# Kernel optimization log

Hardware: AMD Instinct MI355X
Metric: run time of the kernel (lower is better)

Reference implementation:

```python
import jax, jax.numpy as jnp
import numpy as np

D_MODEL = 1024
N_HEADS = 16
HEAD_DIM = D_MODEL // N_HEADS
SCALE = HEAD_DIM ** -0.5
MASK_FILL = -10000.0


def setup_inputs() -> dict:
    key = jax.random.key(0)
    ks = jax.random.split(key, 12)
    B, L, D = 2, 2048, D_MODEL
    inv = 1.0 / np.sqrt(D)
    inp = {
        "query": jax.random.normal(ks[0], (B, L, D), jnp.float32),
        "key": jax.random.normal(ks[1], (B, L, D), jnp.float32),
        "value": jax.random.normal(ks[2], (B, L, D), jnp.float32),
        "Wq": jax.random.normal(ks[3], (D, D), jnp.float32) * inv,
        "bq": jnp.zeros((D,), jnp.float32),
        "Wk": jax.random.normal(ks[4], (D, D), jnp.float32) * inv,
        "bk": jnp.zeros((D,), jnp.float32),
        "Wv": jax.random.normal(ks[5], (D, D), jnp.float32) * inv,
        "bv": jnp.zeros((D,), jnp.float32),
        "Wo": jax.random.normal(ks[6], (D, D), jnp.float32) * inv,
        "bo": jnp.zeros((D,), jnp.float32),
        "valid_mask": jax.random.randint(ks[7], (B, L), 0, 2).astype(jnp.bool_),
    }
    return inp


def reference(query, key, value, Wq, bq, Wk, bk, Wv, bv, Wo, bo, valid_mask):
    B, Lq, D = query.shape
    Lk = key.shape[1]
    H, HD = N_HEADS, HEAD_DIM
    # torch.nn.Linear: y = x @ W.T + b
    Q = (query @ Wq.T + bq).reshape(B, Lq, H, HD).transpose(0, 2, 1, 3)  # [B,H,Lq,HD]
    K = (key @ Wk.T + bk).reshape(B, Lk, H, HD).transpose(0, 2, 1, 3)    # [B,H,Lk,HD]
    V = (value @ Wv.T + bv).reshape(B, Lk, H, HD).transpose(0, 2, 1, 3)  # [B,H,Lk,HD]
    scores = jnp.einsum("bhqd,bhkd->bhqk", Q, K) * SCALE
    scores = jnp.where(valid_mask[:, None, None, :], scores, MASK_FILL)
    weights = jax.nn.softmax(scores, axis=-1)  # dropout is identity at inference
    out = jnp.einsum("bhqk,bhkd->bhqd", weights, V)
    out = out.transpose(0, 2, 1, 3).reshape(B, Lq, D)
    out = out @ Wo.T + bo
    # zero rows of fully-invalid batches
    gate = jnp.any(valid_mask, axis=1).astype(out.dtype)[:, None, None]
    return out * gate
```

## Files before the change

### kernel.cpp

```cpp
#include <hip/hip_runtime.h>
#include <hip/hip_bf16.h>

typedef __hip_bfloat16 bf16;
typedef __attribute__((ext_vector_type(8))) short s8v;
typedef __attribute__((ext_vector_type(4))) float f4v;

#define LOG2E 1.44269504088896340736f
#define CSCALE (0.125f * LOG2E)
#define MASK_B2 (-14426.950408889634f)
#define NEG_BIG (-30000.0f)

#define BB 2
#define LL 2048
#define DD 1024
#define HH 16
#define HD 64
#define MTOT 4096
#define PER_T 4194304

struct alignas(8) B4 { bf16 v[4]; };

__device__ __forceinline__ void async_cp16(const bf16* g, bf16* l) {
    __builtin_amdgcn_global_load_lds(
        (const __attribute__((address_space(1))) void*)g,
        (__attribute__((address_space(3))) void*)l, 16, 0, 0);
}

struct CvtArgs {
    const float* src[7];
    bf16* dst[7];
    int n[7];
};

__global__ __launch_bounds__(256) void cvt_kernel(CvtArgs args) {
    const int which = blockIdx.y;
    const float* __restrict__ src = args.src[which];
    bf16* __restrict__ dst = args.dst[which];
    const int n4 = args.n[which] >> 2;
    const int stride = gridDim.x * 256;
    for (int i = blockIdx.x * 256 + threadIdx.x; i < n4; i += stride) {
        const float4 f = ((const float4*)src)[i];
        B4 o;
        o.v[0] = __float2bfloat16(f.x);
        o.v[1] = __float2bfloat16(f.y);
        o.v[2] = __float2bfloat16(f.z);
        o.v[3] = __float2bfloat16(f.w);
        ((B4*)dst)[i] = o;
    }
}

struct QkvArgs {
    const bf16* A[3];
    const bf16* W[3];
    const float* bias[3];
    bf16* out[3];
};

template <int FUSED>
__global__ __launch_bounds__(256) void gemm128(QkvArgs qa,
                                               const bf16* __restrict__ Ao,
                                               const bf16* __restrict__ Wo_,
                                               const float* __restrict__ bo_,
                                               float* __restrict__ out_f,
                                               const int* __restrict__ mask) {
    __shared__ bf16 sA[128 * 64];
    __shared__ bf16 sB[128 * 64];
    __shared__ int sgate;

    const int which = FUSED ? blockIdx.z : 0;
    const bf16* __restrict__ A = FUSED ? qa.A[which] : Ao;
    const bf16* __restrict__ W = FUSED ? qa.W[which] : Wo_;
    const float* __restrict__ bias = FUSED ? qa.bias[which] : bo_;
    bf16* __restrict__ out_bf = FUSED ? qa.out[which] : nullptr;

    const int lane = threadIdx.x & 63;
    const int w = threadIdx.x >> 6;
    const int lr = lane & 15;
    const int quad = lane >> 4;
    const int wr = w >> 1, wc = w & 1;
    const int rbase = blockIdx.x * 128;
    const int cbase = blockIdx.y * 128;
    const int dma_r = lane >> 3;
    const int dma_cc = ((lane & 7) ^ dma_r) * 8;

    if (!FUSED) {
        if (threadIdx.x == 0) sgate = 0;
        __syncthreads();
        const int b_ = rbase >> 11;
        int any = 0;
        for (int i = threadIdx.x; i < LL; i += 256) any |= mask[b_ * LL + i];
        if (any) sgate = 1;
    }

    f4v acc[4][4] = {};
    for (int kt = 0; kt < DD / 64; kt++) {
        const int k0 = kt * 64;
        __syncthreads();
#pragma unroll
        for (int t = 0; t < 4; t++) {
            const int g = w * 4 + t;
            async_cp16(A + (size_t)(rbase + g * 8 + dma_r) * DD + k0 + dma_cc,
                       &sA[g * 512]);
            async_cp16(W + (size_t)(cbase + g * 8 + dma_r) * DD + k0 + dma_cc,
                       &sB[g * 512]);
        }
        __syncthreads();
#pragma unroll
        for (int s = 0; s < 2; s++) {
            s8v a[4], b[4];
#pragma unroll
            for (int i = 0; i < 4; i++) {
                const int row = wr * 64 + i * 16 + lr;
                a[i] = *(const s8v*)&sA[row * 64 + (((s * 4 + quad) ^ (row & 7)) * 8)];
            }
#pragma unroll
            for (int j = 0; j < 4; j++) {
                const int row = wc * 64 + j * 16 + lr;
                b[j] = *(const s8v*)&sB[row * 64 + (((s * 4 + quad) ^ (row & 7)) * 8)];
            }
#pragma unroll
            for (int i = 0; i < 4; i++)
#pragma unroll
                for (int j = 0; j < 4; j++)
                    acc[i][j] = __builtin_amdgcn_mfma_f32_16x16x32_bf16(a[i], b[j], acc[i][j], 0, 0, 0);
        }
    }

    const float gatef = (!FUSED) ? (sgate ? 1.0f : 0.0f) : 1.0f;

#pragma unroll
    for (int j = 0; j < 4; j++) {
        const int n = cbase + wc * 64 + j * 16 + lr;
        const float bv = bias[n];
#pragma unroll
        for (int i = 0; i < 4; i++) {
#pragma unroll
            for (int r = 0; r < 4; r++) {
                const int m = rbase + wr * 64 + i * 16 + quad * 4 + r;
                const float v = acc[i][j][r] + bv;
                if (!FUSED) {
                    out_f[(size_t)m * DD + n] = v * gatef;
                } else {
                    const int b_ = m >> 11, l = m & (LL - 1);
                    const int h = n >> 6, hd = n & 63;
                    if (which == 2)
                        out_bf[(((size_t)(b_ * HH + h)) * HD + hd) * LL + l] = __float2bfloat16(v);
                    else
                        out_bf[(((size_t)(b_ * HH + h)) * LL + l) * HD + hd] = __float2bfloat16(v);
                }
            }
        }
    }
}

__global__ __launch_bounds__(256) void attn_kernel(const bf16* __restrict__ Q,
                                                   const bf16* __restrict__ K,
                                                   const bf16* __restrict__ Vt,
                                                   const int* __restrict__ mask,
                                                   bf16* __restrict__ Aout) {
    __shared__ bf16 sK[2][64 * 64];
    __shared__ bf16 sV[2][64 * 64];
    __shared__ bf16 sP[4][16 * 72];
    __shared__ float sBias[LL];

    const int lane = threadIdx.x & 63;
    const int w = threadIdx.x >> 6;
    const int lr = lane & 15;
    const int quad = lane >> 4;

    const int bid = blockIdx.x;
    const int qb = bid & 31;
    const int h = (bid >> 5) & 15;
    const int b = bid >> 9;

    const size_t head_off = ((size_t)(b * HH + h)) * LL * HD;
    const bf16* Qh = Q + head_off;
    const bf16* Kh = K + head_off;
    const bf16* Vh = Vt + head_off;
    const int q0 = qb * 64 + w * 16;

    const int dma_r = lane >> 3;
    const int dma_cc = ((lane & 7) ^ dma_r) * 8;
    const int sw = lr & 7;

    {
        const int* mb = mask + b * LL;
        for (int i = threadIdx.x; i < LL; i += 256)
            sBias[i] = mb[i] ? 0.0f : MASK_B2;
#pragma unroll
        for (int t = 0; t < 2; t++) {
            const int g = w * 2 + t;
            async_cp16(Kh + (size_t)(g * 8 + dma_r) * HD + dma_cc, &sK[0][g * 512]);
            async_cp16(Vh + (size_t)(g * 8 + dma_r) * LL + dma_cc, &sV[0][g * 512]);
        }
    }
    __syncthreads();

    const s8v aq0 = *(const s8v*)(Qh + (size_t)(q0 + lr) * HD + quad * 8);
    const s8v aq1 = *(const s8v*)(Qh + (size_t)(q0 + lr) * HD + 32 + quad * 8);

    bf16* sPw = &sP[w][0];
    f4v O[4] = {};
    float mrun = NEG_BIG, lrun = 0.0f;

    int asrc[4];
#pragma unroll
    for (int r = 0; r < 4; r++) asrc[r] = (lane & 48) | (quad * 4 + r);

    for (int kt = 0; kt < LL / 64; kt++) {
        const int kbase = kt * 64;
        const bf16* kb = &sK[kt & 1][0];
        const bf16* vb = &sV[kt & 1][0];

        if (kt < LL / 64 - 1) {
            const int nb = (kt + 1) & 1;
#pragma unroll
            for (int t = 0; t < 2; t++) {
                const int g = w * 2 + t;
                async_cp16(Kh + (size_t)(kbase + 64 + g * 8 + dma_r) * HD + dma_cc,
                           &sK[nb][g * 512]);
                async_cp16(Vh + (size_t)(g * 8 + dma_r) * LL + kbase + 64 + dma_cc,
                           &sV[nb][g * 512]);
            }
        }

        f4v T[4];
#pragma unroll
        for (int j = 0; j < 4; j++) {
            const int row = 16 * j + lr;
            const s8v kb0 = *(const s8v*)&kb[row * 64 + ((quad ^ sw) * 8)];
            const s8v kb1 = *(const s8v*)&kb[row * 64 + (((quad + 4) ^ sw) * 8)];
            f4v t = {};
            t = __builtin_amdgcn_mfma_f32_16x16x32_bf16(kb0, aq0, t, 0, 0, 0);
            T[j] = __builtin_amdgcn_mfma_f32_16x16x32_bf16(kb1, aq1, t, 0, 0, 0);
        }

        s8v v0[4], v1[4];
#pragma unroll
        for (int dt = 0; dt < 4; dt++) {
            const int vrow = dt * 16 + lr;
            v0[dt] = *(const s8v*)&vb[vrow * 64 + ((quad ^ sw) * 8)];
            v1[dt] = *(const s8v*)&vb[vrow * 64 + (((quad + 4) ^ sw) * 8)];
        }

        float mloc = NEG_BIG;
#pragma unroll
        for (int j = 0; j < 4; j++) {
            const f4v bj = *(const f4v*)&sBias[kbase + j * 16 + quad * 4];
#pragma unroll
            for (int r = 0; r < 4; r++) {
                T[j][r] = T[j][r] * CSCALE + bj[r];
                mloc = fmaxf(mloc, T[j][r]);
            }
        }
        mloc = fmaxf(mloc, __shfl_xor(mloc, 16));
        mloc = fmaxf(mloc, __shfl_xor(mloc, 32));

        if (__any(mloc > mrun)) {
            const float mnew = fmaxf(mrun, mloc);
            const float alphaq = exp2f(mrun - mnew);
            mrun = mnew;
            lrun *= alphaq;
            float aB[4];
#pragma unroll
            for (int r = 0; r < 4; r++) aB[r] = __shfl(alphaq, asrc[r]);
#pragma unroll
            for (int dt = 0; dt < 4; dt++)
#pragma unroll
                for (int r = 0; r < 4; r++) O[dt][r] *= aB[r];
        }

        float ls = 0.0f;
#pragma unroll
        for (int j = 0; j < 4; j++)
#pragma unroll
            for (int r = 0; r < 4; r++) {
                const float e = exp2f(T[j][r] - mrun);
                T[j][r] = e;
                ls += e;
            }
        ls += __shfl_xor(ls, 16);
        ls += __shfl_xor(ls, 32);
        lrun += ls;

        asm volatile("" ::: "memory");
#pragma unroll
        for (int j = 0; j < 4; j++) {
            B4 pk;
            pk.v[0] = __float2bfloat16(T[j][0]);
            pk.v[1] = __float2bfloat16(T[j][1]);
            pk.v[2] = __float2bfloat16(T[j][2]);
            pk.v[3] = __float2bfloat16(T[j][3]);
            *(B4*)&sPw[lr * 72 + j * 16 + quad * 4] = pk;
        }
        asm volatile("s_waitcnt lgkmcnt(0)" ::: "memory");
        const s8v pa0 = *(const s8v*)(sPw + lr * 72 + quad * 8);
        const s8v pa1 = *(const s8v*)(sPw + lr * 72 + 32 + quad * 8);

#pragma unroll
        for (int dt = 0; dt < 4; dt++) {
            O[dt] = __builtin_amdgcn_mfma_f32_16x16x32_bf16(pa0, v0[dt], O[dt], 0, 0, 0);
            O[dt] = __builtin_amdgcn_mfma_f32_16x16x32_bf16(pa1, v1[dt], O[dt], 0, 0, 0);
        }

        __syncthreads();
    }

    const float linv = 1.0f / lrun;
    float lB[4];
#pragma unroll
    for (int r = 0; r < 4; r++) lB[r] = __shfl(linv, asrc[r]);
#pragma unroll
    for (int dt = 0; dt < 4; dt++)
#pragma unroll
        for (int r = 0; r < 4; r++) {
            const int q = q0 + quad * 4 + r;
            Aout[((size_t)(b * LL + q)) * DD + h * HD + dt * 16 + lr] =
                __float2bfloat16(O[dt][r] * lB[r]);
        }
}

extern "C" void kernel_launch(void* const* d_in, const int* in_sizes, int n_in,
                              void* d_out, int out_size, void* d_ws, size_t ws_size,
                              hipStream_t stream) {
    const float* query = (const float*)d_in[0];
    const float* key   = (const float*)d_in[1];
    const float* value = (const float*)d_in[2];
    const float* Wq = (const float*)d_in[3];
    const float* bq = (const float*)d_in[4];
    const float* Wk = (const float*)d_in[5];
    const float* bk = (const float*)d_in[6];
    const float* Wv = (const float*)d_in[7];
    const float* bv = (const float*)d_in[8];
    const float* Wo = (const float*)d_in[9];
    const float* bo = (const float*)d_in[10];
    const int* mask = (const int*)d_in[11];

    bf16* base = (bf16*)d_ws;
    bf16* qx = base;
    bf16* kx = qx + PER_T;
    bf16* vx = kx + PER_T;
    bf16* wq = vx + PER_T;
    bf16* wk = wq + DD * DD;
    bf16* wv = wk + DD * DD;
    bf16* wo = wv + DD * DD;
    bf16* Qs = wo + DD * DD;
    bf16* Ks = Qs + PER_T;
    bf16* Vst = Ks + PER_T;
    bf16* aws = Vst + PER_T;

    CvtArgs ca;
    ca.src[0] = query; ca.dst[0] = qx; ca.n[0] = PER_T;
    ca.src[1] = key;   ca.dst[1] = kx; ca.n[1] = PER_T;
    ca.src[2] = value; ca.dst[2] = vx; ca.n[2] = PER_T;
    ca.src[3] = Wq;    ca.dst[3] = wq; ca.n[3] = DD * DD;
    ca.src[4] = Wk;    ca.dst[4] = wk; ca.n[4] = DD * DD;
    ca.src[5] = Wv;    ca.dst[5] = wv; ca.n[5] = DD * DD;
    ca.src[6] = Wo;    ca.dst[6] = wo; ca.n[6] = DD * DD;
    cvt_kernel<<<dim3(1024, 7), 256, 0, stream>>>(ca);

    QkvArgs qa;
    qa.A[0] = qx; qa.W[0] = wq; qa.bias[0] = bq; qa.out[0] = Qs;
    qa.A[1] = kx; qa.W[1] = wk; qa.bias[1] = bk; qa.out[1] = Ks;
    qa.A[2] = vx; qa.W[2] = wv; qa.bias[2] = bv; qa.out[2] = Vst;

    gemm128<1><<<dim3(MTOT / 128, DD / 128, 3), 256, 0, stream>>>(
        qa, nullptr, nullptr, nullptr, nullptr, nullptr);

    attn_kernel<<<BB * HH * (LL / 64), 256, 0, stream>>>(Qs, Ks, Vst, mask, aws);

    QkvArgs dummy{};
    gemm128<0><<<dim3(MTOT / 128, DD / 128, 1), 256, 0, stream>>>(
        dummy, aws, wo, bo, (float*)d_out, mask);
}
```

Before: 293.6 us.

## Split attention keys across waves with register-resident P and smaller output GEMM tiles

The attention kernel now has each wave handle all 64 queries against a 16-key slice of every key tile, instead of 16 queries against all keys. Probabilities stay in registers and feed 16x16x16 MFMAs directly, removing the shared-memory round trip for P. The per-wave softmax states are merged at the end through shared memory using LDS atomics before writing bf16 output. The output projection GEMM switches to 64-row tiles to launch more blocks, at the cost of more accumulators per wave in attention and an extra reduction step.

```diff
diff --git a/kernel.cpp b/kernel.cpp
--- a/kernel.cpp
+++ b/kernel.cpp
@@ -3,6 +3,7 @@
 
 typedef __hip_bfloat16 bf16;
 typedef __attribute__((ext_vector_type(8))) short s8v;
+typedef __attribute__((ext_vector_type(4))) short s4v;
 typedef __attribute__((ext_vector_type(4))) float f4v;
 
 #define LOG2E 1.44269504088896340736f
@@ -24,6 +25,16 @@
     __builtin_amdgcn_global_load_lds(
         (const __attribute__((address_space(1))) void*)g,
         (__attribute__((address_space(3))) void*)l, 16, 0, 0);
+}
+
+__device__ __forceinline__ f4v mfma16x16x16bf(s4v a, s4v b, f4v c) {
+    return __builtin_amdgcn_mfma_f32_16x16x16bf16_1k(a, b, c, 0, 0, 0);
+}
+
+__device__ __forceinline__ unsigned pk2(float lo, float hi) {
+    unsigned a = __builtin_bit_cast(unsigned, hi) + 0x8000u;
+    unsigned b = __builtin_bit_cast(unsigned, lo) + 0x8000u;
+    return __builtin_amdgcn_perm(a, b, 0x07060302u);
 }
 
 struct CvtArgs {
@@ -56,16 +67,17 @@
     bf16* out[3];
 };
 
-template <int FUSED>
+template <int FUSED, int MT>
 __global__ __launch_bounds__(256) void gemm128(QkvArgs qa,
                                                const bf16* __restrict__ Ao,
                                                const bf16* __restrict__ Wo_,
                                                const float* __restrict__ bo_,
                                                float* __restrict__ out_f,
                                                const int* __restrict__ mask) {
-    __shared__ bf16 sA[128 * 64];
+    __shared__ bf16 sA[MT * 64];
     __shared__ bf16 sB[128 * 64];
     __shared__ int sgate;
+    constexpr int NI = MT / 32;
 
     const int which = FUSED ? blockIdx.z : 0;
     const bf16* __restrict__ A = FUSED ? qa.A[which] : Ao;
@@ -78,7 +90,7 @@
     const int lr = lane & 15;
     const int quad = lane >> 4;
     const int wr = w >> 1, wc = w & 1;
-    const int rbase = blockIdx.x * 128;
+    const int rbase = blockIdx.x * MT;
     const int cbase = blockIdx.y * 128;
     const int dma_r = lane >> 3;
     const int dma_cc = ((lane & 7) ^ dma_r) * 8;
@@ -92,25 +104,29 @@
         if (any) sgate = 1;
     }
 
-    f4v acc[4][4] = {};
+    f4v acc[NI][4] = {};
     for (int kt = 0; kt < DD / 64; kt++) {
         const int k0 = kt * 64;
         __syncthreads();
 #pragma unroll
+        for (int t = 0; t < NI; t++) {
+            const int g = w * NI + t;
+            async_cp16(A + (size_t)(rbase + g * 8 + dma_r) * DD + k0 + dma_cc,
+                       &sA[g * 512]);
+        }
+#pragma unroll
         for (int t = 0; t < 4; t++) {
             const int g = w * 4 + t;
-            async_cp16(A + (size_t)(rbase + g * 8 + dma_r) * DD + k0 + dma_cc,
-                       &sA[g * 512]);
             async_cp16(W + (size_t)(cbase + g * 8 + dma_r) * DD + k0 + dma_cc,
                        &sB[g * 512]);
         }
         __syncthreads();
 #pragma unroll
         for (int s = 0; s < 2; s++) {
-            s8v a[4], b[4];
-#pragma unroll
-            for (int i = 0; i < 4; i++) {
-                const int row = wr * 64 + i * 16 + lr;
+            s8v a[NI], b[4];
+#pragma unroll
+            for (int i = 0; i < NI; i++) {
+                const int row = wr * (MT / 2) + i * 16 + lr;
                 a[i] = *(const s8v*)&sA[row * 64 + (((s * 4 + quad) ^ (row & 7)) * 8)];
             }
 #pragma unroll
@@ -119,7 +135,7 @@
                 b[j] = *(const s8v*)&sB[row * 64 + (((s * 4 + quad) ^ (row & 7)) * 8)];
             }
 #pragma unroll
-            for (int i = 0; i < 4; i++)
+            for (int i = 0; i < NI; i++)
 #pragma unroll
                 for (int j = 0; j < 4; j++)
                     acc[i][j] = __builtin_amdgcn_mfma_f32_16x16x32_bf16(a[i], b[j], acc[i][j], 0, 0, 0);
@@ -133,10 +149,10 @@
         const int n = cbase + wc * 64 + j * 16 + lr;
         const float bv = bias[n];
 #pragma unroll
-        for (int i = 0; i < 4; i++) {
+        for (int i = 0; i < NI; i++) {
 #pragma unroll
             for (int r = 0; r < 4; r++) {
-                const int m = rbase + wr * 64 + i * 16 + quad * 4 + r;
+                const int m = rbase + wr * (MT / 2) + i * 16 + quad * 4 + r;
                 const float v = acc[i][j][r] + bv;
                 if (!FUSED) {
                     out_f[(size_t)m * DD + n] = v * gatef;
@@ -153,15 +169,14 @@
     }
 }
 
-__global__ __launch_bounds__(256) void attn_kernel(const bf16* __restrict__ Q,
-                                                   const bf16* __restrict__ K,
-                                                   const bf16* __restrict__ Vt,
-                                                   const int* __restrict__ mask,
-                                                   bf16* __restrict__ Aout) {
-    __shared__ bf16 sK[2][64 * 64];
-    __shared__ bf16 sV[2][64 * 64];
-    __shared__ bf16 sP[4][16 * 72];
+__global__ __launch_bounds__(256, 3) void attn_kernel(const bf16* __restrict__ Q,
+                                                      const bf16* __restrict__ K,
+                                                      const bf16* __restrict__ Vt,
+                                                      const int* __restrict__ mask,
+                                                      bf16* __restrict__ Aout) {
+    __shared__ bf16 sKV[2][2][64 * 64];
     __shared__ float sBias[LL];
+    __shared__ float sML[4][4][2][16];
 
     const int lane = threadIdx.x & 63;
     const int w = threadIdx.x >> 6;
@@ -177,11 +192,10 @@
     const bf16* Qh = Q + head_off;
     const bf16* Kh = K + head_off;
     const bf16* Vh = Vt + head_off;
-    const int q0 = qb * 64 + w * 16;
+    const int q0 = qb * 64;
 
     const int dma_r = lane >> 3;
     const int dma_cc = ((lane & 7) ^ dma_r) * 8;
-    const int sw = lr & 7;
 
     {
         const int* mb = mask + b * LL;
@@ -190,134 +204,171 @@
 #pragma unroll
         for (int t = 0; t < 2; t++) {
             const int g = w * 2 + t;
-            async_cp16(Kh + (size_t)(g * 8 + dma_r) * HD + dma_cc, &sK[0][g * 512]);
-            async_cp16(Vh + (size_t)(g * 8 + dma_r) * LL + dma_cc, &sV[0][g * 512]);
+            async_cp16(Kh + (size_t)(g * 8 + dma_r) * HD + dma_cc, &sKV[0][0][g * 512]);
+            async_cp16(Vh + (size_t)(g * 8 + dma_r) * LL + dma_cc, &sKV[0][1][g * 512]);
         }
     }
     __syncthreads();
 
-    const s8v aq0 = *(const s8v*)(Qh + (size_t)(q0 + lr) * HD + quad * 8);
-    const s8v aq1 = *(const s8v*)(Qh + (size_t)(q0 + lr) * HD + 32 + quad * 8);
-
-    bf16* sPw = &sP[w][0];
-    f4v O[4] = {};
-    float mrun = NEG_BIG, lrun = 0.0f;
-
+    s8v Qf[4][2];
+#pragma unroll
+    for (int j = 0; j < 4; j++)
+#pragma unroll
+        for (int c = 0; c < 2; c++)
+            Qf[j][c] = *(const s8v*)(Qh + (size_t)(q0 + j * 16 + lr) * HD + c * 32 + quad * 8);
+
+    f4v O[4][4] = {};
+    float m[4], l[4];
+#pragma unroll
+    for (int j = 0; j < 4; j++) { m[j] = NEG_BIG; l[j] = 0.0f; }
+
+    const int krow = w * 16 + lr;
+    const int ksw = lr & 7;
+    const int vchunkbase = w * 2 + (quad >> 1);
+    const int vsub = (quad & 1) * 4;
     int asrc[4];
 #pragma unroll
     for (int r = 0; r < 4; r++) asrc[r] = (lane & 48) | (quad * 4 + r);
 
     for (int kt = 0; kt < LL / 64; kt++) {
-        const int kbase = kt * 64;
-        const bf16* kb = &sK[kt & 1][0];
-        const bf16* vb = &sV[kt & 1][0];
+        const int kb = kt * 64;
+        const bf16* kb_ = &sKV[kt & 1][0][0];
+        const bf16* vb_ = &sKV[kt & 1][1][0];
 
         if (kt < LL / 64 - 1) {
             const int nb = (kt + 1) & 1;
 #pragma unroll
             for (int t = 0; t < 2; t++) {
                 const int g = w * 2 + t;
-                async_cp16(Kh + (size_t)(kbase + 64 + g * 8 + dma_r) * HD + dma_cc,
-                           &sK[nb][g * 512]);
-                async_cp16(Vh + (size_t)(g * 8 + dma_r) * LL + kbase + 64 + dma_cc,
-                           &sV[nb][g * 512]);
+                async_cp16(Kh + (size_t)(kb + 64 + g * 8 + dma_r) * HD + dma_cc,
+                           &sKV[nb][0][g * 512]);
+                async_cp16(Vh + (size_t)(g * 8 + dma_r) * LL + kb + 64 + dma_cc,
+                           &sKV[nb][1][g * 512]);
             }
         }
 
+        const s8v kf0 = *(const s8v*)&kb_[krow * 64 + ((quad ^ ksw) * 8)];
+        const s8v kf1 = *(const s8v*)&kb_[krow * 64 + (((4 + quad) ^ ksw) * 8)];
         f4v T[4];
 #pragma unroll
         for (int j = 0; j < 4; j++) {
-            const int row = 16 * j + lr;
-            const s8v kb0 = *(const s8v*)&kb[row * 64 + ((quad ^ sw) * 8)];
-            const s8v kb1 = *(const s8v*)&kb[row * 64 + (((quad + 4) ^ sw) * 8)];
             f4v t = {};
-            t = __builtin_amdgcn_mfma_f32_16x16x32_bf16(kb0, aq0, t, 0, 0, 0);
-            T[j] = __builtin_amdgcn_mfma_f32_16x16x32_bf16(kb1, aq1, t, 0, 0, 0);
-        }
-
-        s8v v0[4], v1[4];
+            t = __builtin_amdgcn_mfma_f32_16x16x32_bf16(kf0, Qf[j][0], t, 0, 0, 0);
+            T[j] = __builtin_amdgcn_mfma_f32_16x16x32_bf16(kf1, Qf[j][1], t, 0, 0, 0);
+        }
+
+        s4v vf[4];
 #pragma unroll
         for (int dt = 0; dt < 4; dt++) {
             const int vrow = dt * 16 + lr;
-            v0[dt] = *(const s8v*)&vb[vrow * 64 + ((quad ^ sw) * 8)];
-            v1[dt] = *(const s8v*)&vb[vrow * 64 + (((quad + 4) ^ sw) * 8)];
-        }
-
-        float mloc = NEG_BIG;
+            vf[dt] = *(const s4v*)&vb_[vrow * 64 + ((vchunkbase ^ (lr & 7)) * 8) + vsub];
+        }
+
+        const f4v bj = *(const f4v*)&sBias[kb + w * 16 + quad * 4];
+        float mloc[4], mnew[4];
 #pragma unroll
         for (int j = 0; j < 4; j++) {
-            const f4v bj = *(const f4v*)&sBias[kbase + j * 16 + quad * 4];
-#pragma unroll
-            for (int r = 0; r < 4; r++) {
-                T[j][r] = T[j][r] * CSCALE + bj[r];
-                mloc = fmaxf(mloc, T[j][r]);
+#pragma unroll
+            for (int r = 0; r < 4; r++) T[j][r] = T[j][r] * CSCALE + bj[r];
+            float v = fmaxf(fmaxf(T[j][0], T[j][1]), fmaxf(T[j][2], T[j][3]));
+            v = fmaxf(v, __shfl_xor(v, 16));
+            v = fmaxf(v, __shfl_xor(v, 32));
+            mloc[j] = v;
+            mnew[j] = fmaxf(m[j], v);
+        }
+
+        const bool upd = (mnew[0] > m[0]) | (mnew[1] > m[1]) |
+                         (mnew[2] > m[2]) | (mnew[3] > m[3]);
+        if (__any(upd)) {
+#pragma unroll
+            for (int j = 0; j < 4; j++) {
+                const float alpha = __builtin_amdgcn_exp2f(m[j] - mnew[j]);
+                m[j] = mnew[j];
+                l[j] *= alpha;
+#pragma unroll
+                for (int r = 0; r < 4; r++) {
+                    const float aB = __shfl(alpha, asrc[r]);
+                    O[j][0][r] *= aB; O[j][1][r] *= aB;
+                    O[j][2][r] *= aB; O[j][3][r] *= aB;
+                }
             }
         }
-        mloc = fmaxf(mloc, __shfl_xor(mloc, 16));
-        mloc = fmaxf(mloc, __shfl_xor(mloc, 32));
-
-        if (__any(mloc > mrun)) {
-            const float mnew = fmaxf(mrun, mloc);
-            const float alphaq = exp2f(mrun - mnew);
-            mrun = mnew;
-            lrun *= alphaq;
-            float aB[4];
-#pragma unroll
-            for (int r = 0; r < 4; r++) aB[r] = __shfl(alphaq, asrc[r]);
+
+        s4v P[4];
+#pragma unroll
+        for (int j = 0; j < 4; j++) {
+            float e0 = __builtin_amdgcn_exp2f(T[j][0] - m[j]);
+            float e1 = __builtin_amdgcn_exp2f(T[j][1] - m[j]);
+            float e2 = __builtin_amdgcn_exp2f(T[j][2] - m[j]);
+            float e3 = __builtin_amdgcn_exp2f(T[j][3] - m[j]);
+            float ls = (e0 + e1) + (e2 + e3);
+            ls += __shfl_xor(ls, 16);
+            ls += __shfl_xor(ls, 32);
+            l[j] += ls;
+            const unsigned u01 = pk2(e0, e1);
+            const unsigned u23 = pk2(e2, e3);
+            int2 pi = make_int2((int)u01, (int)u23);
+            P[j] = __builtin_bit_cast(s4v, pi);
+        }
+
+#pragma unroll
+        for (int j = 0; j < 4; j++)
 #pragma unroll
             for (int dt = 0; dt < 4; dt++)
-#pragma unroll
-                for (int r = 0; r < 4; r++) O[dt][r] *= aB[r];
-        }
-
-        float ls = 0.0f;
-#pragma unroll
-        for (int j = 0; j < 4; j++)
-#pragma unroll
-            for (int r = 0; r < 4; r++) {
-                const float e = exp2f(T[j][r] - mrun);
-                T[j][r] = e;
-                ls += e;
-            }
-        ls += __shfl_xor(ls, 16);
-        ls += __shfl_xor(ls, 32);
-        lrun += ls;
-
-        asm volatile("" ::: "memory");
+                O[j][dt] = mfma16x16x16bf(P[j], vf[dt], O[j][dt]);
+
+        __syncthreads();
+    }
+
+    if (lane < 16) {
 #pragma unroll
         for (int j = 0; j < 4; j++) {
-            B4 pk;
-            pk.v[0] = __float2bfloat16(T[j][0]);
-            pk.v[1] = __float2bfloat16(T[j][1]);
-            pk.v[2] = __float2bfloat16(T[j][2]);
-            pk.v[3] = __float2bfloat16(T[j][3]);
-            *(B4*)&sPw[lr * 72 + j * 16 + quad * 4] = pk;
-        }
-        asm volatile("s_waitcnt lgkmcnt(0)" ::: "memory");
-        const s8v pa0 = *(const s8v*)(sPw + lr * 72 + quad * 8);
-        const s8v pa1 = *(const s8v*)(sPw + lr * 72 + 32 + quad * 8);
-
-#pragma unroll
-        for (int dt = 0; dt < 4; dt++) {
-            O[dt] = __builtin_amdgcn_mfma_f32_16x16x32_bf16(pa0, v0[dt], O[dt], 0, 0, 0);
-            O[dt] = __builtin_amdgcn_mfma_f32_16x16x32_bf16(pa1, v1[dt], O[dt], 0, 0, 0);
-        }
-
-        __syncthreads();
-    }
-
-    const float linv = 1.0f / lrun;
-    float lB[4];
-#pragma unroll
-    for (int r = 0; r < 4; r++) lB[r] = __shfl(linv, asrc[r]);
-#pragma unroll
-    for (int dt = 0; dt < 4; dt++)
+            sML[j][w][0][lane] = m[j];
+            sML[j][w][1][lane] = l[j];
+        }
+    }
+    float* R = (float*)&sKV[0][0][0];
+    {
+        f4v z = {};
+        for (int i = threadIdx.x; i < 64 * 68 / 4; i += 256) ((f4v*)R)[i] = z;
+    }
+    __syncthreads();
+
+#pragma unroll
+    for (int j = 0; j < 4; j++) {
+        float mg = NEG_BIG, lg = 0.0f;
+        float mw[4], lw[4];
+#pragma unroll
+        for (int ww = 0; ww < 4; ww++) {
+            mw[ww] = sML[j][ww][0][lr];
+            lw[ww] = sML[j][ww][1][lr];
+            mg = fmaxf(mg, mw[ww]);
+        }
+#pragma unroll
+        for (int ww = 0; ww < 4; ww++) lg += lw[ww] * __builtin_amdgcn_exp2f(mw[ww] - mg);
+        const float sc = __builtin_amdgcn_exp2f(m[j] - mg) / lg;
 #pragma unroll
         for (int r = 0; r < 4; r++) {
-            const int q = q0 + quad * 4 + r;
-            Aout[((size_t)(b * LL + q)) * DD + h * HD + dt * 16 + lr] =
-                __float2bfloat16(O[dt][r] * lB[r]);
-        }
+            const float f = __shfl(sc, asrc[r]);
+            const int row = j * 16 + quad * 4 + r;
+#pragma unroll
+            for (int dt = 0; dt < 4; dt++)
+                atomicAdd(&R[row * 68 + dt * 16 + lr], O[j][dt][r] * f);
+        }
+    }
+    __syncthreads();
+
+    {
+        const int qloc = w * 16 + (lane >> 2);
+        const int dbase = (lane & 3) * 16;
+        bf16* dst = Aout + ((size_t)(b * LL + q0 + qloc)) * DD + h * HD + dbase;
+#pragma unroll
+        for (int c = 0; c < 4; c++) {
+            const f4v x = *(const f4v*)&R[qloc * 68 + dbase + c * 4];
+            int2 o = make_int2((int)pk2(x[0], x[1]), (int)pk2(x[2], x[3]));
+            *(int2*)(dst + c * 4) = o;
+        }
+    }
 }
 
 extern "C" void kernel_launch(void* const* d_in, const int* in_sizes, int n_in,
@@ -364,12 +415,12 @@
     qa.A[1] = kx; qa.W[1] = wk; qa.bias[1] = bk; qa.out[1] = Ks;
     qa.A[2] = vx; qa.W[2] = wv; qa.bias[2] = bv; qa.out[2] = Vst;
 
-    gemm128<1><<<dim3(MTOT / 128, DD / 128, 3), 256, 0, stream>>>(
+    gemm128<1, 128><<<dim3(MTOT / 128, DD / 128, 3), 256, 0, stream>>>(
         qa, nullptr, nullptr, nullptr, nullptr, nullptr);
 
     attn_kernel<<<BB * HH * (LL / 64), 256, 0, stream>>>(Qs, Ks, Vst, mask, aws);
 
     QkvArgs dummy{};
-    gemm128<0><<<dim3(MTOT / 128, DD / 128, 1), 256, 0, stream>>>(
+    gemm128<0, 64><<<dim3(MTOT / 64, DD / 128, 1), 256, 0, stream>>>(
         dummy, aws, wo, bo, (float*)d_out, mask);
 }
```

Measured after the change: 382.6 us. 30.3% more time.
